# Optimization experiments

Measured on AMD Instinct MI355X. Metric: run time of the kernel, lower is better.

The kernel has to match this reference:

```python
import jax, jax.numpy as jnp
import numpy as np
from jax import lax

# SSD300/COCO geometry
B, P, C = 16, 8732, 81
V_CENTER, V_SIZE = 0.1, 0.2        # box coder variances
SCORE_THRESH = 0.05
NMS_THRESH = 0.45
DETS_PER_IMG = 100
PRE_NMS_TOPK = 1000                # fixed-size candidate set for jit-compatible NMS
MIN_SIZE = 0.01                    # remove_small_boxes threshold


def setup_inputs() -> dict:
    key = jax.random.key(0)
    k1, k2, k3, k4, k5 = jax.random.split(key, 5)
    # scale logits so a realistic fraction of softmax scores clears SCORE_THRESH
    pred_logits = jax.random.normal(k1, (B, P, C), jnp.float32) * 2.0
    pred_boxes = jax.random.normal(k2, (B, P, 4), jnp.float32) * 0.5
    # priors in (cx, cy, w, h), normalized coords, positive sizes
    cxcy = jax.random.uniform(k3, (P, 2), jnp.float32, 0.05, 0.95)
    wh = jax.random.uniform(k4, (P, 2), jnp.float32, 0.02, 0.4)
    priors = jnp.concatenate([cxcy, wh], axis=-1)
    target_sizes = jax.random.randint(k5, (B, 2), 480, 1333)  # (h, w) per image
    return {"pred_logits": pred_logits, "pred_boxes": pred_boxes,
            "priors": priors, "target_sizes": target_sizes}


def _decode(rel, priors):
    # SSD box coder: rel = (dx, dy, dw, dh), priors = (cx, cy, w, h) -> xyxy
    cxcy = priors[:, :2] + rel[:, :2] * V_CENTER * priors[:, 2:]
    wh = priors[:, 2:] * jnp.exp(rel[:, 2:] * V_SIZE)
    return jnp.concatenate([cxcy - 0.5 * wh, cxcy + 0.5 * wh], axis=-1)


def _pairwise_iou(b):
    # b: [K, 4] xyxy
    area = (b[:, 2] - b[:, 0]) * (b[:, 3] - b[:, 1])
    lt = jnp.maximum(b[:, None, :2], b[None, :, :2])
    rb = jnp.minimum(b[:, None, 2:], b[None, :, 2:])
    whi = jnp.clip(rb - lt, 0.0)
    inter = whi[..., 0] * whi[..., 1]
    return inter / (area[:, None] + area[None, :] - inter + 1e-9)


def _per_image(logits, rel, priors, size_hw):
    nc1 = C - 1  # foreground classes
    # decode and scale to pixel coords: target_size.flip(0).repeat(2) = [w, h, w, h]
    size_hw = size_hw.astype(jnp.float32)
    whwh = jnp.concatenate([size_hw[::-1], size_hw[::-1]])
    boxes = _decode(rel, priors) * whwh                     # [P, 4]
    scores = jax.nn.softmax(logits, axis=-1)[:, 1:]          # [P, C-1], drop background
    # score threshold + remove_small_boxes, fused as a mask (jit-safe)
    size_ok = ((boxes[:, 2] - boxes[:, 0]) >= MIN_SIZE) & \
              ((boxes[:, 3] - boxes[:, 1]) >= MIN_SIZE)      # [P]
    valid = (scores > SCORE_THRESH) & size_ok[:, None]       # [P, C-1]
    s_flat = jnp.where(valid, scores, -1.0).reshape(-1)      # [P*(C-1)]
    vals, idx = lax.top_k(s_flat, PRE_NMS_TOPK)
    prior_idx = idx // nc1
    labels_k = idx % nc1 + 1                                 # class ids in [1, C)
    boxes_k = boxes[prior_idx]                               # [K, 4]
    vmask = vals > 0.0                                       # real candidates
    # batched_nms via per-class coordinate offset
    max_coord = jnp.max(jnp.where(vmask[:, None], boxes_k, 0.0))
    offs_boxes = boxes_k + (labels_k.astype(jnp.float32) * (max_coord + 1.0))[:, None]
    iou = _pairwise_iou(offs_boxes)                          # [K, K]
    cols = jnp.arange(PRE_NMS_TOPK)

    def body(i, keep):
        suppress = (iou[i] > NMS_THRESH) & keep[i] & (cols > i)
        return keep & ~suppress

    keep = lax.fori_loop(0, PRE_NMS_TOPK, body, vmask)
    kept_scores = jnp.where(keep, vals, -1.0)
    fvals, fidx = lax.top_k(kept_scores, DETS_PER_IMG)
    fvalid = fvals > 0.0
    out_boxes = jnp.where(fvalid[:, None], boxes_k[fidx], 0.0)
    out_scores = jnp.where(fvalid, fvals, 0.0)
    out_labels = jnp.where(fvalid, labels_k[fidx], -1)
    return out_boxes, out_scores, out_labels


def reference(pred_logits, pred_boxes, priors, target_sizes):
    boxes, scores, labels = jax.vmap(_per_image, in_axes=(0, 0, None, 0))(
        pred_logits, pred_boxes, priors, target_sizes)
    # padded, fixed-size equivalent of the per-image list of dicts
    return boxes, scores, labels
```

## Files before the change

kernel.cpp:

```cpp
#include <hip/hip_runtime.h>
#include <math.h>

#pragma clang fp contract(off)

#define NIMG 16
#define NP   8732
#define NCLS 81
#define NFG  80
#define KTOP 1000
#define KPAD 1024
#define DETS 100
#define CAPMAX 166912
#define BASEBITS 0x3D000000u
#define CNT_STRIDE 64
#define TILEB 137
#define NB 640

#define OFF_BOXES  0u
#define OFF_CNT    2235392u
#define OFF_GHIST  2239488u
#define OFF_CSCORE 2280448u
#define OFF_CLABEL 2345984u
#define OFF_CBOX   2411520u
#define OFF_COFFS  2673664u
#define OFF_CAREA  2935808u
#define OFF_VALIDW 3001344u
#define OFF_MASK   3003392u
#define OFF_CAND   5100544u
#define MEMSET_LEN 45056u

typedef unsigned long long u64;
typedef unsigned int u32;

#define AS_GLOBAL __attribute__((address_space(1)))
#define AS_LOCAL  __attribute__((address_space(3)))

__global__ __launch_bounds__(256, 6) void k_decode(
    const float* __restrict__ logits, const float* __restrict__ rel,
    const float* __restrict__ priors, const int* __restrict__ tsz,
    float* __restrict__ boxes_out, u64* __restrict__ cand,
    u32* __restrict__ cnt, u32* __restrict__ ghist, int cap)
{
#pragma clang fp contract(off)
    __shared__ __align__(16) float lx[64 * NCLS];
    __shared__ float pmx[4 * 64];
    __shared__ float psm[4 * 64];
    __shared__ u32 sok[64];
    __shared__ u32 lhist[NB];
    int b  = blockIdx.x & 15;
    int g  = blockIdx.x >> 4;
    int p0 = g * 64;
    int t  = threadIdx.x;
    int lane = t & 63;
    int q = t >> 6;
    int npri = NP - p0; if (npri > 64) npri = 64;
    int words = npri * NCLS;

    const u32* s32 = (const u32*)(logits + ((size_t)b * NP + p0) * NCLS);
    u32* lxw = (u32*)lx;
    int full = words >> 8;
    for (int k = q; k < full; k += 4)
        __builtin_amdgcn_global_load_lds(
            (AS_GLOBAL const u32*)(s32 + (k << 8) + (lane << 2)),
            (AS_LOCAL u32*)(lxw + (k << 8)), 16, 0, 0);
    int base = full << 8;
    int c4 = (words - base) >> 6;
    for (int k = q; k < c4; k += 4)
        __builtin_amdgcn_global_load_lds(
            (AS_GLOBAL const u32*)(s32 + base + (k << 6) + lane),
            (AS_LOCAL u32*)(lxw + base + (k << 6)), 4, 0, 0);
    int base2 = base + (c4 << 6);
    if (q == 0 && lane < words - base2) lxw[base2 + lane] = s32[base2 + lane];

    for (int i = t; i < NB; i += 256) lhist[i] = 0;

    int p = p0 + lane;
    bool active = p < NP;

    if (q == 0) {
        u32 ok = 0;
        if (active) {
            float4 pr = ((const float4*)priors)[p];
            float4 rl = ((const float4*)rel)[(size_t)b * NP + p];
            float W = (float)tsz[b * 2 + 1], H = (float)tsz[b * 2 + 0];
            float cx = pr.x + (rl.x * 0.1f) * pr.z;
            float cy = pr.y + (rl.y * 0.1f) * pr.w;
            float w_ = pr.z * expf(rl.z * 0.2f);
            float h_ = pr.w * expf(rl.w * 0.2f);
            float4 bx;
            bx.x = (cx - 0.5f * w_) * W; bx.y = (cy - 0.5f * h_) * H;
            bx.z = (cx + 0.5f * w_) * W; bx.w = (cy + 0.5f * h_) * H;
            ((float4*)boxes_out)[(size_t)b * NP + p] = bx;
            ok = ((bx.z - bx.x) >= 0.01f) && ((bx.w - bx.y) >= 0.01f);
        }
        sok[lane] = ok;
    }
    __syncthreads();

    int tb = lane * NCLS;
    int nk = (q == 0) ? 21 : 20;
    float x[21];
    #pragma unroll
    for (int k = 0; k < 21; ++k) {
        int c = q + 4 * k;
        x[k] = (k < nk) ? lx[tb + c] : -3.4e38f;
    }
    float pm = -3.4e38f;
    #pragma unroll
    for (int k = 0; k < 21; ++k) if (k < nk) pm = fmaxf(pm, x[k]);
    pmx[q * 64 + lane] = pm;
    __syncthreads();
    float m = fmaxf(fmaxf(pmx[lane], pmx[64 + lane]),
                    fmaxf(pmx[128 + lane], pmx[192 + lane]));

    float ps = 0.f;
    #pragma unroll
    for (int k = 0; k < 21; ++k) {
        if (k < nk) { x[k] = expf(x[k] - m); ps += x[k]; }
    }
    psm[q * 64 + lane] = ps;
    __syncthreads();
    float s = (psm[lane] + psm[64 + lane]) + (psm[128 + lane] + psm[192 + lane]);

    float hi = 0.05000075f * s;
    float lo = 0.04999925f * s;
    u32 pass = 0, band = 0;
    u32 sizeok = sok[lane];
    if (active && sizeok) {
        #pragma unroll
        for (int k = 0; k < 21; ++k) {
            int c = q + 4 * k;
            if (k < nk && c >= 1) {
                bool pa = x[k] > hi;
                bool bd = (!pa) && (x[k] > lo);
                pass |= ((u32)pa) << k;
                band |= ((u32)bd) << k;
            }
        }
    }
    while (band) {
        int k = __builtin_ctz(band); band &= band - 1;
        int c = q + 4 * k;
        float e = expf(lx[tb + c] - m);
        if (e / s > 0.05f) pass |= 1u << k;
    }
    int cnt_t = __popc(pass);

    int pre = cnt_t;
    #pragma unroll
    for (int d = 1; d < 64; d <<= 1) {
        int o = __shfl_up(pre, d);
        if (lane >= d) pre += o;
    }
    u32 wbase = 0;
    if (lane == 63 && pre > 0)
        wbase = atomicAdd(cnt + b * CNT_STRIDE, (u32)pre);
    wbase = (u32)__shfl((int)wbase, 63);
    u32 pos = wbase + (u32)(pre - cnt_t);

    u64* cb = cand + (size_t)b * cap;
    u32 flatneg = 0xFFFFFFFFu - (u32)p * NFG;
    while (pass) {
        int k = __builtin_ctz(pass); pass &= pass - 1;
        int c = q + 4 * k;
        float e = expf(lx[tb + c] - m);
        float d = e / s;
        if ((int)pos < cap) {
            u32 sb = __float_as_uint(d);
            cb[pos] = ((u64)sb << 32) | (u64)(flatneg - (u32)(c - 1));
            u32 bin = (sb - BASEBITS) >> 16; if (bin > NB - 1) bin = NB - 1;
            atomicAdd(&lhist[bin], 1u);
        }
        ++pos;
    }
    __syncthreads();
    u32* gh = ghist + b * NB;
    for (int i = t; i < NB; i += 256) {
        u32 v = lhist[i];
        if (v) atomicAdd(gh + i, v);
    }
}

__device__ __forceinline__ void suffix_find(
    u32* hist, u32* wt, u32 K, int tid,
    volatile int* outI, volatile u32* outNext)
{
    int lane = tid & 63, w = tid >> 6;
    u32 v[8]; u32 tot = 0;
    #pragma unroll
    for (int k = 0; k < 8; ++k) { v[k] = hist[tid * 8 + k]; tot += v[k]; }
    u32 ws = tot;
    #pragma unroll
    for (int d = 1; d < 64; d <<= 1) {
        u32 o = __shfl_down(ws, d);
        if (lane + d < 64) ws += o;
    }
    if (lane == 0) wt[w] = ws;
    __syncthreads();
    u32 tail = 0;
    for (int w2 = w + 1; w2 < 16; ++w2) tail += wt[w2];
    u32 after = (ws - tot) + tail;
    u32 sufk[9];
    sufk[8] = after;
    #pragma unroll
    for (int k = 7; k >= 0; --k) sufk[k] = v[k] + sufk[k + 1];
    #pragma unroll
    for (int k = 0; k < 8; ++k) {
        if (sufk[k] >= K && sufk[k + 1] < K) {
            *outI = tid * 8 + k;
            *outNext = sufk[k + 1];
        }
    }
    __syncthreads();
}

__global__ __launch_bounds__(1024) void k_select(
    const u64* __restrict__ cand, const u32* __restrict__ cnt,
    const u32* __restrict__ ghist, const float* __restrict__ boxes,
    float* __restrict__ cscore, int* __restrict__ clabel,
    float4* __restrict__ cbox, float4* __restrict__ coffs,
    float* __restrict__ carea, u64* __restrict__ validw, int cap)
{
#pragma clang fp contract(off)
    __shared__ u32 h[NB];
    __shared__ u32 fh[8192];
    __shared__ u32 wt[16];
    __shared__ u64 buf[2048];
    __shared__ float red16[16];
    __shared__ int sh_c, sh_i2;
    __shared__ u32 sh_S, sh_next, sh_d, sh_m;
    int b = blockIdx.x, t = threadIdx.x, lane = t & 63;
    u32 n = min(cnt[b * CNT_STRIDE], (u32)cap);
    const u64* cb = cand + (size_t)b * cap;
    const float4* cb4 = (const float4*)cb;

    float4 cur[4]; bool unused_cq;
    #pragma unroll
    for (int e = 0; e < 4; ++e) {
        u32 p2 = (u32)(e << 10) + (u32)t;
        cur[e] = make_float4(0.f, 0.f, 0.f, 0.f);
        if ((p2 << 1) < n) cur[e] = cb4[p2];
    }
    (void)unused_cq;

    for (int i = t; i < NB; i += 1024) h[i] = ghist[b * NB + i];
    if (t == 0) { sh_c = -2; sh_i2 = -2; sh_S = 0; sh_next = 0; sh_m = 0; }
    __syncthreads();
    if (t < 64) {
        u32 v[10]; u32 tot = 0;
        #pragma unroll
        for (int k = 0; k < 10; ++k) { v[k] = h[t * 10 + k]; tot += v[k]; }
        u32 ws = tot;
        #pragma unroll
        for (int d = 1; d < 64; d <<= 1) {
            u32 o = (u32)__shfl_down((int)ws, d);
            if (t + d < 64) ws += o;
        }
        u32 suf[11];
        suf[10] = ws - tot;
        #pragma unroll
        for (int k = 9; k >= 0; --k) suf[k] = v[k] + suf[k + 1];
        #pragma unroll
        for (int k = 0; k < 10; ++k) {
            if (suf[k] >= (u32)KTOP && suf[k + 1] < (u32)KTOP) {
                sh_c = t * 10 + k; sh_S = suf[k]; sh_next = suf[k + 1];
            }
        }
    }
    __syncthreads();
    int c = sh_c;
    u32 T = 0;
    if (c >= 0) {
        u32 Tc = BASEBITS + ((u32)c << 16);
        if (sh_S <= 2048u) {
            T = Tc;
        } else {
            u32 nhi = sh_next;
            for (int i = t; i < 8192; i += 1024) fh[i] = 0;
            __syncthreads();
            for (u32 i = (u32)t; i < n; i += 1024) {
                u32 sb = (u32)(cb[i] >> 32);
                if ((sb & 0xFFFF0000u) == Tc)
                    atomicAdd(&fh[(sb >> 3) & 0x1FFFu], 1u);
            }
            __syncthreads();
            suffix_find(fh, wt, (u32)KTOP - nhi, t, &sh_i2, &sh_d);
            T = (sh_i2 >= 0) ? (Tc + ((u32)sh_i2 << 3)) : Tc;
        }
    }
    for (u32 bs0 = 0; bs0 < n; bs0 += 8192) {
        u32 bs1 = bs0 + 8192;
        float4 nxt[4];
        if (bs1 < n) {
            #pragma unroll
            for (int e = 0; e < 4; ++e) {
                u32 p2 = (bs1 >> 1) + (u32)(e << 10) + (u32)t;
                nxt[e] = make_float4(0.f, 0.f, 0.f, 0.f);
                if ((p2 << 1) < n) nxt[e] = cb4[p2];
            }
        } else {
            #pragma unroll
            for (int e = 0; e < 4; ++e) nxt[e] = make_float4(0.f, 0.f, 0.f, 0.f);
        }
        #pragma unroll
        for (int e = 0; e < 4; ++e) {
            u32 gk = bs0 + (((u32)(e << 10) + (u32)t) << 1);
            u64 k0 = ((u64)__float_as_uint(cur[e].y) << 32) | (u64)__float_as_uint(cur[e].x);
            u64 k1 = ((u64)__float_as_uint(cur[e].w) << 32) | (u64)__float_as_uint(cur[e].z);
            bool pick0 = (gk < n)     && ((u32)(k0 >> 32) >= T);
            bool pick1 = (gk + 1 < n) && ((u32)(k1 >> 32) >= T);
            u64 bal0 = __ballot(pick0);
            u32 wb = 0;
            if (lane == 0 && bal0) wb = atomicAdd(&sh_m, (u32)__popcll(bal0));
            wb = (u32)__shfl((int)wb, 0);
            if (pick0) {
                u32 pos = wb + (u32)__popcll(bal0 & ((1ULL << lane) - 1ULL));
                if (pos < 2048) buf[pos] = k0;
            }
            u64 bal1 = __ballot(pick1);
            u32 wb1 = 0;
            if (lane == 0 && bal1) wb1 = atomicAdd(&sh_m, (u32)__popcll(bal1));
            wb1 = (u32)__shfl((int)wb1, 0);
            if (pick1) {
                u32 pos = wb1 + (u32)__popcll(bal1 & ((1ULL << lane) - 1ULL));
                if (pos < 2048) buf[pos] = k1;
            }
        }
        #pragma unroll
        for (int e = 0; e < 4; ++e) cur[e] = nxt[e];
    }
    __syncthreads();
    u32 m = min(sh_m, 2048u);
    for (int i = t; i < 2048; i += 1024) if ((u32)i >= m) buf[i] = 0ULL;
    __syncthreads();
    for (int k = 2; k <= 2048; k <<= 1) {
        for (int j = k >> 1; j >= 64; j >>= 1) {
            #pragma unroll
            for (int e = 0; e < 2; ++e) {
                int i = t + e * 1024;
                int ixj = i ^ j;
                if (ixj > i) {
                    u64 a = buf[i], bb = buf[ixj];
                    bool up = (i & k) == 0;
                    if (up ? (a < bb) : (a > bb)) { buf[i] = bb; buf[ixj] = a; }
                }
            }
            __syncthreads();
        }
        u64 v0 = buf[t], v1 = buf[t + 1024];
        bool up0 = (t & k) == 0;
        bool up1 = ((t + 1024) & k) == 0;
        int js = ((k >> 1) < 32) ? (k >> 1) : 32;
        for (int j = js; j >= 1; j >>= 1) {
            u64 o0 = __shfl_xor(v0, j);
            u64 o1 = __shfl_xor(v1, j);
            bool lo0 = (t & j) == 0;
            v0 = (lo0 == up0) ? (v0 > o0 ? v0 : o0) : (v0 < o0 ? v0 : o0);
            v1 = (lo0 == up1) ? (v1 > o1 ? v1 : o1) : (v1 < o1 ? v1 : o1);
        }
        buf[t] = v0; buf[t + 1024] = v1;
        __syncthreads();
    }
    u64 key = (t < KTOP) ? buf[t] : 0ULL;
    float s = __uint_as_float((u32)(key >> 32));
    bool valid = s > 0.0f;
    u32 flat = valid ? (0xFFFFFFFFu - (u32)key) : 0u;
    int prior = (int)(flat / NFG);
    int cls = (int)(flat - (u32)prior * NFG) + 1;
    float4 bx = make_float4(0.f, 0.f, 0.f, 0.f);
    if (valid) bx = ((const float4*)boxes)[b * NP + prior];
    cscore[b * KPAD + t] = s;
    clabel[b * KPAD + t] = cls;
    cbox[b * KPAD + t] = bx;
    u64 vb = __ballot(valid);
    if (lane == 0) validw[b * 16 + (t >> 6)] = vb;
    float lm = valid ? fmaxf(fmaxf(bx.x, bx.y), fmaxf(bx.z, bx.w)) : 0.0f;
    lm = fmaxf(lm, 0.0f);
    #pragma unroll
    for (int d = 1; d < 64; d <<= 1) lm = fmaxf(lm, __shfl_xor(lm, d));
    if (lane == 0) red16[t >> 6] = lm;
    __syncthreads();
    float mc = red16[0];
    #pragma unroll
    for (int w = 1; w < 16; ++w) mc = fmaxf(mc, red16[w]);
    float off = (float)cls * (mc + 1.0f);
    float4 ob = valid ? make_float4(bx.x + off, bx.y + off, bx.z + off, bx.w + off)
                      : make_float4(0.f, 0.f, 0.f, 0.f);
    float area = valid ? (ob.z - ob.x) * (ob.w - ob.y) : 0.0f;
    coffs[b * KPAD + t] = ob;
    carea[b * KPAD + t] = area;
}

__global__ __launch_bounds__(1024) void k_iou(
    const float4* __restrict__ coffs, const float* __restrict__ carea,
    u64* __restrict__ cmask)
{
#pragma clang fp contract(off)
    __shared__ float4 bs[KPAD];
    __shared__ float as_[KPAD];
    int b = blockIdx.x & 15, tile = blockIdx.x >> 4;
    int t = threadIdx.x;
    bs[t] = coffs[b * KPAD + t];
    as_[t] = carea[b * KPAD + t];
    __syncthreads();
    int j = tile * 64 + (t & 63);
    int w = t >> 6;
    float4 bj = bs[j];
    float aj = as_[j];
    int r0 = w * 64;
    u64 bits = 0;
    #pragma unroll 4
    for (int k = 0; k < 64; ++k) {
        int r = r0 + k;
        float4 br = bs[r];
        float ar = as_[r];
        float ltx = fmaxf(br.x, bj.x), lty = fmaxf(br.y, bj.y);
        float rbx = fminf(br.z, bj.z), rby = fminf(br.w, bj.w);
        float wx = fmaxf(rbx - ltx, 0.0f), wy = fmaxf(rby - lty, 0.0f);
        float inter = wx * wy;
        float denom = ((ar + aj) - inter) + 1e-9f;
        float iou = inter / denom;
        bool sup = (iou > 0.45f) && (j > r);
        bits |= ((u64)sup) << k;
    }
    cmask[((size_t)b * 16 + w) * KPAD + j] = bits;
}

__global__ __launch_bounds__(1024) void k_nms(
    const u64* __restrict__ cmask, const u64* __restrict__ validw,
    const float* __restrict__ cscore, const int* __restrict__ clabel,
    const float4* __restrict__ cbox, float* __restrict__ out)
{
    __shared__ __align__(16) u64 smask[16 * KPAD];
    __shared__ u64 sk[16];
    __shared__ int pfx[17];
    __shared__ int slot[DETS];
    int b = blockIdx.x, t = threadIdx.x, lane = t & 63;

    {
        const float4* cm4 = (const float4*)(cmask + (size_t)b * 16 * KPAD);
        float4* sm4 = (float4*)smask;
        #pragma unroll
        for (int i = 0; i < 8; ++i) sm4[t + (i << 10)] = cm4[t + (i << 10)];
    }
    __syncthreads();

    if (t < 64) {
        u64 kept[16];
        #pragma unroll
        for (int g = 0; g < 16; ++g) {
            u64 vg = validw[b * 16 + g];
            bool rem = false;
            #pragma unroll
            for (int w2 = 0; w2 < 16; ++w2)
                if (w2 < g)
                    rem |= (kept[w2] & smask[w2 * KPAD + g * 64 + lane]) != 0ULL;
            u64 cg = smask[g * KPAD + g * 64 + lane];
            bool myv = ((vg >> lane) & 1ULL) && !rem;
            u64 K = __ballot(myv);
            for (;;) {
                u64 K2 = __ballot(myv && ((K & cg) == 0ULL));
                if (K2 == K) break;
                K = K2;
            }
            kept[g] = K;
        }
        if (lane == 0) {
            int run = 0;
            #pragma unroll
            for (int l = 0; l < 16; ++l) {
                sk[l] = kept[l]; pfx[l] = run; run += __popcll(kept[l]);
            }
            pfx[16] = run;
        }
    }
    __syncthreads();
    if (t < 16) {
        int r = pfx[t];
        u64 wv = sk[t];
        while (wv && r < DETS) {
            int bit = __builtin_ctzll(wv);
            slot[r] = t * 64 + bit;
            ++r;
            wv &= wv - 1;
        }
    }
    __syncthreads();
    int total = min(pfx[16], DETS);
    if (t < DETS) {
        int r = t;
        float4 bx = make_float4(0.f, 0.f, 0.f, 0.f);
        float s = 0.0f;
        int lb = -1;
        if (r < total) {
            int cdx = slot[r];
            bx = cbox[b * KPAD + cdx];
            s = cscore[b * KPAD + cdx];
            lb = clabel[b * KPAD + cdx];
        }
        float* ob = out + ((size_t)b * DETS + r) * 4;
        ob[0] = bx.x; ob[1] = bx.y; ob[2] = bx.z; ob[3] = bx.w;
        out[NIMG * DETS * 4 + b * DETS + r] = s;
        out[NIMG * DETS * 4 + NIMG * DETS + b * DETS + r] = (float)lb;
    }
}

extern "C" void kernel_launch(void* const* d_in, const int* in_sizes, int n_in,
                              void* d_out, int out_size, void* d_ws, size_t ws_size,
                              hipStream_t stream) {
    const float* logits = (const float*)d_in[0];
    const float* rel    = (const float*)d_in[1];
    const float* priors = (const float*)d_in[2];
    const int*   tsz    = (const int*)d_in[3];
    float* out = (float*)d_out;
    char* ws = (char*)d_ws;

    float* boxes  = (float*)(ws + OFF_BOXES);
    u32*   cnt    = (u32*)(ws + OFF_CNT);
    u32*   ghist  = (u32*)(ws + OFF_GHIST);
    float* cscore = (float*)(ws + OFF_CSCORE);
    int*   clabel = (int*)(ws + OFF_CLABEL);
    float4* cbox  = (float4*)(ws + OFF_CBOX);
    float4* coffs = (float4*)(ws + OFF_COFFS);
    float* carea  = (float*)(ws + OFF_CAREA);
    u64*   validw = (u64*)(ws + OFF_VALIDW);
    u64*   cmask  = (u64*)(ws + OFF_MASK);
    u64*   cand   = (u64*)(ws + OFF_CAND);

    long long avail = ((long long)ws_size - (long long)OFF_CAND) / (NIMG * 8);
    int cap = (int)(avail < CAPMAX ? (avail > 0 ? avail : 1) : CAPMAX);
    cap &= ~1;

    hipMemsetAsync(cnt, 0, MEMSET_LEN, stream);
    k_decode<<<NIMG * TILEB, 256, 0, stream>>>(logits, rel, priors, tsz,
                                               boxes, cand, cnt, ghist, cap);
    k_select<<<NIMG, 1024, 0, stream>>>(cand, cnt, ghist, boxes, cscore, clabel,
                                        cbox, coffs, carea, validw, cap);
    k_iou<<<NIMG * 16, 1024, 0, stream>>>(coffs, carea, cmask);
    k_nms<<<NIMG, 1024, 0, stream>>>(cmask, validw, cscore, clabel, cbox, out);
}
```

Before: 154.8 us.

## Refine top-k threshold to sort 1024 candidates instead of 2048 in select

In k_select, when the coarse histogram threshold leaves between 1024 and 2048 candidates, a second finer histogram over the threshold bin is built so the candidate set can be compacted to at most 1024 entries. The bitonic sort then runs over 1024 keys with one element per thread instead of 2048, which removes the sort stages and barriers that handle the larger set. In k_nms, the per-group valid words are loaded once into registers and broadcast with shuffles instead of being read from global memory inside the loop. The price is an extra histogram, prefix-scan and compaction pass with additional barriers, plus more code complexity around the fallback path.

Measured after the change: 146.6 us. 1.06x faster.

```diff
diff --git a/kernel.cpp b/kernel.cpp
--- a/kernel.cpp
+++ b/kernel.cpp
@@ -223,25 +223,24 @@
 {
 #pragma clang fp contract(off)
     __shared__ u32 h[NB];
-    __shared__ u32 fh[8192];
+    __shared__ __align__(16) u32 fh[8192];
     __shared__ u32 wt[16];
     __shared__ u64 buf[2048];
     __shared__ float red16[16];
-    __shared__ int sh_c, sh_i2;
-    __shared__ u32 sh_S, sh_next, sh_d, sh_m;
+    __shared__ int sh_c, sh_i2, sh_f;
+    __shared__ u32 sh_S, sh_next, sh_d, sh_m, sh_S2, sh_m2;
     int b = blockIdx.x, t = threadIdx.x, lane = t & 63;
     u32 n = min(cnt[b * CNT_STRIDE], (u32)cap);
     const u64* cb = cand + (size_t)b * cap;
     const float4* cb4 = (const float4*)cb;
 
-    float4 cur[4]; bool unused_cq;
+    float4 cur[4];
     #pragma unroll
     for (int e = 0; e < 4; ++e) {
         u32 p2 = (u32)(e << 10) + (u32)t;
         cur[e] = make_float4(0.f, 0.f, 0.f, 0.f);
         if ((p2 << 1) < n) cur[e] = cb4[p2];
     }
-    (void)unused_cq;
 
     for (int i = t; i < NB; i += 1024) h[i] = ghist[b * NB + i];
     if (t == 0) { sh_c = -2; sh_i2 = -2; sh_S = 0; sh_next = 0; sh_m = 0; }
@@ -270,10 +269,12 @@
     __syncthreads();
     int c = sh_c;
     u32 T = 0;
+    bool common_path = false;
     if (c >= 0) {
         u32 Tc = BASEBITS + ((u32)c << 16);
         if (sh_S <= 2048u) {
             T = Tc;
+            common_path = true;
         } else {
             u32 nhi = sh_next;
             for (int i = t; i < 8192; i += 1024) fh[i] = 0;
@@ -333,33 +334,118 @@
     u32 m = min(sh_m, 2048u);
     for (int i = t; i < 2048; i += 1024) if ((u32)i >= m) buf[i] = 0ULL;
     __syncthreads();
-    for (int k = 2; k <= 2048; k <<= 1) {
-        for (int j = k >> 1; j >= 64; j >>= 1) {
+
+    int sortn = 2048;
+    if (m <= 1024u) {
+        sortn = 1024;
+    } else if (common_path) {
+        u32 nhi = sh_next;
+        u32 K2 = (u32)KTOP - nhi;
+        u32 cbin = (BASEBITS >> 16) + (u32)c;
+        for (int i = t; i < 2048; i += 1024) fh[i] = 0;
+        if (t == 0) { sh_f = -1; sh_S2 = 0; sh_m2 = 0; }
+        __syncthreads();
+        u64 a0 = buf[t], a1 = buf[t + 1024];
+        u32 s0 = (u32)(a0 >> 32), s1 = (u32)(a1 >> 32);
+        if ((s0 >> 16) == cbin) atomicAdd(&fh[(s0 >> 5) & 0x7FFu], 1u);
+        if ((s1 >> 16) == cbin) atomicAdd(&fh[(s1 >> 5) & 0x7FFu], 1u);
+        __syncthreads();
+        {
+            int l2 = t & 63, w2 = t >> 6;
+            u32 v0b = fh[t * 2], v1b = fh[t * 2 + 1];
+            u32 tot = v0b + v1b;
+            u32 ws = tot;
             #pragma unroll
-            for (int e = 0; e < 2; ++e) {
-                int i = t + e * 1024;
+            for (int d = 1; d < 64; d <<= 1) {
+                u32 o = (u32)__shfl_down((int)ws, d);
+                if (l2 + d < 64) ws += o;
+            }
+            if (l2 == 0) wt[w2] = ws;
+            __syncthreads();
+            u32 tail = 0;
+            for (int ww = w2 + 1; ww < 16; ++ww) tail += wt[ww];
+            u32 after = (ws - tot) + tail;
+            u32 suf1 = v1b + after;
+            u32 suf0 = v0b + suf1;
+            if (suf0 >= K2 && suf1 < K2)  { sh_f = t * 2;     sh_S2 = suf0; }
+            if (suf1 >= K2 && after < K2) { sh_f = t * 2 + 1; sh_S2 = suf1; }
+        }
+        __syncthreads();
+        if (sh_f >= 0 && nhi + sh_S2 <= 1024u) {
+            u32 T2 = (cbin << 16) | ((u32)sh_f << 5);
+            u64* buf2 = (u64*)fh;
+            bool p0 = (s0 >= T2);
+            bool p1 = (s1 >= T2);
+            u64 bal = __ballot(p0);
+            u32 wb = 0;
+            if (lane == 0 && bal) wb = atomicAdd(&sh_m2, (u32)__popcll(bal));
+            wb = (u32)__shfl((int)wb, 0);
+            if (p0) buf2[wb + (u32)__popcll(bal & ((1ULL << lane) - 1ULL))] = a0;
+            bal = __ballot(p1);
+            wb = 0;
+            if (lane == 0 && bal) wb = atomicAdd(&sh_m2, (u32)__popcll(bal));
+            wb = (u32)__shfl((int)wb, 0);
+            if (p1) buf2[wb + (u32)__popcll(bal & ((1ULL << lane) - 1ULL))] = a1;
+            __syncthreads();
+            u32 m2 = sh_m2;
+            buf[t] = (t < (int)m2) ? buf2[t] : 0ULL;
+            sortn = 1024;
+            __syncthreads();
+        }
+    }
+
+    if (sortn == 1024) {
+        for (int k = 2; k <= 1024; k <<= 1) {
+            for (int j = k >> 1; j >= 64; j >>= 1) {
+                int i = t;
                 int ixj = i ^ j;
                 if (ixj > i) {
                     u64 a = buf[i], bb = buf[ixj];
                     bool up = (i & k) == 0;
                     if (up ? (a < bb) : (a > bb)) { buf[i] = bb; buf[ixj] = a; }
                 }
-            }
+                __syncthreads();
+            }
+            u64 v0 = buf[t];
+            bool up0 = (t & k) == 0;
+            int js = ((k >> 1) < 32) ? (k >> 1) : 32;
+            for (int j = js; j >= 1; j >>= 1) {
+                u64 o0 = __shfl_xor(v0, j);
+                bool lo0 = (t & j) == 0;
+                v0 = (lo0 == up0) ? (v0 > o0 ? v0 : o0) : (v0 < o0 ? v0 : o0);
+            }
+            buf[t] = v0;
             __syncthreads();
         }
-        u64 v0 = buf[t], v1 = buf[t + 1024];
-        bool up0 = (t & k) == 0;
-        bool up1 = ((t + 1024) & k) == 0;
-        int js = ((k >> 1) < 32) ? (k >> 1) : 32;
-        for (int j = js; j >= 1; j >>= 1) {
-            u64 o0 = __shfl_xor(v0, j);
-            u64 o1 = __shfl_xor(v1, j);
-            bool lo0 = (t & j) == 0;
-            v0 = (lo0 == up0) ? (v0 > o0 ? v0 : o0) : (v0 < o0 ? v0 : o0);
-            v1 = (lo0 == up1) ? (v1 > o1 ? v1 : o1) : (v1 < o1 ? v1 : o1);
-        }
-        buf[t] = v0; buf[t + 1024] = v1;
-        __syncthreads();
+    } else {
+        for (int k = 2; k <= 2048; k <<= 1) {
+            for (int j = k >> 1; j >= 64; j >>= 1) {
+                #pragma unroll
+                for (int e = 0; e < 2; ++e) {
+                    int i = t + e * 1024;
+                    int ixj = i ^ j;
+                    if (ixj > i) {
+                        u64 a = buf[i], bb = buf[ixj];
+                        bool up = (i & k) == 0;
+                        if (up ? (a < bb) : (a > bb)) { buf[i] = bb; buf[ixj] = a; }
+                    }
+                }
+                __syncthreads();
+            }
+            u64 v0 = buf[t], v1 = buf[t + 1024];
+            bool up0 = (t & k) == 0;
+            bool up1 = ((t + 1024) & k) == 0;
+            int js = ((k >> 1) < 32) ? (k >> 1) : 32;
+            for (int j = js; j >= 1; j >>= 1) {
+                u64 o0 = __shfl_xor(v0, j);
+                u64 o1 = __shfl_xor(v1, j);
+                bool lo0 = (t & j) == 0;
+                v0 = (lo0 == up0) ? (v0 > o0 ? v0 : o0) : (v0 < o0 ? v0 : o0);
+                v1 = (lo0 == up1) ? (v1 > o1 ? v1 : o1) : (v1 < o1 ? v1 : o1);
+            }
+            buf[t] = v0; buf[t + 1024] = v1;
+            __syncthreads();
+        }
     }
     u64 key = (t < KTOP) ? buf[t] : 0ULL;
     float s = __uint_as_float((u32)(key >> 32));
@@ -437,6 +523,9 @@
     __shared__ int slot[DETS];
     int b = blockIdx.x, t = threadIdx.x, lane = t & 63;
 
+    u64 vw_reg = 0;
+    if (t < 16) vw_reg = validw[b * 16 + t];
+
     {
         const float4* cm4 = (const float4*)(cmask + (size_t)b * 16 * KPAD);
         float4* sm4 = (float4*)smask;
@@ -449,7 +538,7 @@
         u64 kept[16];
         #pragma unroll
         for (int g = 0; g < 16; ++g) {
-            u64 vg = validw[b * 16 + g];
+            u64 vg = (u64)__shfl((long long)vw_reg, g);
             bool rem = false;
             #pragma unroll
             for (int w2 = 0; w2 < 16; ++w2)
```
